# Kernel optimization log

Measured on AMD Instinct MI355X. Metric: run time of the kernel, lower is better.

The kernel has to match this reference:

```python
import jax, jax.numpy as jnp
import numpy as np

B, D0, D1, D2 = 512, 4096, 4096, 4096
W_SCALE = 0.01  # small init so sigmoids stay in a useful range


def setup_inputs() -> dict:
    key = jax.random.key(0)
    k0, k1, k2, k3, k4 = jax.random.split(key, 5)
    return {
        "data": jax.random.uniform(k0, (B, D0), dtype=jnp.float32),
        "W1": jax.random.normal(k1, (D0, D1), dtype=jnp.float32) * W_SCALE,
        "W2": jax.random.normal(k2, (D1, D2), dtype=jnp.float32) * W_SCALE,
        "b1": jax.random.normal(k3, (D1,), dtype=jnp.float32),
        "b2": jax.random.normal(k4, (D2,), dtype=jnp.float32),
        "iterations": 10,
    }


def reference(data, W1, W2, b1, b2, iterations):
    """Mean-field conditional sample of a 3-layer DBM (visible clamped to data).

    Faithful to conditional_sample_general_meanfield with mean_cond (sigmoid
    of bias + interaction), sample_state[0]=False, invtemperature=1.0.
    Schedule per iteration: odd layers (j=1) then even layers (j=2).
    """
    beta = jnp.float32(1.0)
    nb = data.shape[0]
    # initial states: layer mean activations broadcast over the batch
    s1 = jnp.broadcast_to(jax.nn.sigmoid(b1), (nb, b1.shape[0]))
    s2 = jnp.broadcast_to(jax.nn.sigmoid(b2), (nb, b2.shape[0]))

    def gibbs_step(carry, _):
        s1, s2 = carry
        # j=1: interaction from below (gradOutput: data @ W1) and above (gradInput: s2 @ W2^T)
        s1 = jax.nn.sigmoid(b1 + beta * (data @ W1 + s2 @ W2.T))
        # j=2: interaction from below (gradOutput: s1 @ W2); j=0 clamped
        s2 = jax.nn.sigmoid(b2 + beta * (s1 @ W2))
        return (s1, s2), None

    (s1, s2), _ = jax.lax.scan(gibbs_step, (s1, s2), None, length=iterations)
    # original returns [state0, state1, state2]; state0 == data (clamped)
    return jnp.stack([s1, s2])  # [2, B, D]
```

## Files before the change

### kernel.cpp

```cpp
#include <hip/hip_runtime.h>


typedef __bf16 bf16_t;
typedef __attribute__((ext_vector_type(8))) __bf16 bf16x8;
typedef __attribute__((ext_vector_type(4))) float f32x4;
typedef __attribute__((ext_vector_type(2))) _Float16 half2v;

typedef const __attribute__((address_space(1))) void* gptr_t;
typedef __attribute__((address_space(3))) void* lptr_t;

constexpr int M = 512, N = 4096, K = 4096;
constexpr int BM = 128, BN = 128, BK = 32, SUB = 2;
constexpr int SPLIT = 4;
constexpr int PHASES = K / (SPLIT * BK * SUB);
constexpr int NTILES = (M / BM) * (N / BN);
constexpr int TILE_H2 = BM * BN / 2;


__global__ __launch_bounds__(256) void prep_w(const float* __restrict__ in,
                                              bf16_t* __restrict__ outT,
                                              bf16_t* __restrict__ outC) {
  __shared__ float tile[32][65];
  const int tid = threadIdx.x;
  const int x0 = blockIdx.x * 32;
  const int y0 = blockIdx.y * 64;
  const int tx = tid & 31, ty = tid >> 5;
#pragma unroll
  for (int i = 0; i < 8; ++i)
    tile[tx][ty + 8 * i] = in[(size_t)(y0 + ty + 8 * i) * 4096 + x0 + tx];
  __syncthreads();
  {
    const int rr = tid >> 3, seg = tid & 7;
    bf16x8 v;
#pragma unroll
    for (int j = 0; j < 8; ++j) v[j] = (bf16_t)tile[rr][seg * 8 + j];
    *(bf16x8*)(outT + (size_t)(x0 + rr) * 4096 + y0 + seg * 8) = v;
  }
  if (outC) {
    const int yy = tid >> 2, seg = tid & 3;
    bf16x8 v;
#pragma unroll
    for (int j = 0; j < 8; ++j) v[j] = (bf16_t)tile[seg * 8 + j][yy];
    *(bf16x8*)(outC + (size_t)(y0 + yy) * 4096 + x0 + seg * 8) = v;
  }
}

__global__ __launch_bounds__(256) void cvt_bf16(const float* __restrict__ in,
                                                bf16_t* __restrict__ out) {
  const size_t i8 = ((size_t)blockIdx.x * 256 + threadIdx.x) * 8;
  float4 a = *(const float4*)(in + i8);
  float4 b = *(const float4*)(in + i8 + 4);
  bf16x8 o;
  o[0] = (bf16_t)a.x; o[1] = (bf16_t)a.y; o[2] = (bf16_t)a.z; o[3] = (bf16_t)a.w;
  o[4] = (bf16_t)b.x; o[5] = (bf16_t)b.y; o[6] = (bf16_t)b.z; o[7] = (bf16_t)b.w;
  *(bf16x8*)(out + i8) = o;
}

__global__ __launch_bounds__(256) void init_s2(const float* __restrict__ b2,
                                               bf16_t* __restrict__ s2, int total) {
  int i = blockIdx.x * 256 + threadIdx.x;
  if (i < total) {
    float x = b2[i & (N - 1)];
    s2[i] = (bf16_t)(1.0f / (1.0f + __expf(-x)));
  }
}

__global__ __launch_bounds__(256, 2) void gemm_bt(
    const bf16_t* __restrict__ A,
    const bf16_t* __restrict__ BT,
    _Float16* __restrict__ slabs) {
  __shared__ __align__(16) bf16_t sA[2 * SUB * BM * BK];
  __shared__ __align__(16) bf16_t sB[2 * SUB * BN * BK];

  const int tid = threadIdx.x;
  const int wid = tid >> 6;
  const int l   = tid & 63;
  const int r   = l & 15;
  const int q   = l >> 4;
  const int wm  = wid & 1;
  const int wn  = wid >> 1;

  const int m0 = blockIdx.y * BM;
  const int n0 = blockIdx.x * BN;
  const int z  = blockIdx.z;
  const int tile = blockIdx.y * gridDim.x + blockIdx.x;

  const bf16_t* Ab = A + (size_t)m0 * K + (size_t)z * (PHASES * SUB * BK);
  const bf16_t* Bb = BT + (size_t)n0 * K + (size_t)z * (PHASES * SUB * BK);

  const int srow = l >> 2;
  const int scol = (l & 3) * 8;

  f32x4 acc[4][4];
  const f32x4 zero = {0.0f, 0.0f, 0.0f, 0.0f};
#pragma unroll
  for (int i = 0; i < 4; ++i)
#pragma unroll
    for (int j = 0; j < 4; ++j) acc[i][j] = zero;

  auto issue = [&](int ph, int pb) {
    const size_t kof = (size_t)ph * (SUB * BK);
#pragma unroll
    for (int s = 0; s < SUB; ++s) {
#pragma unroll
      for (int cc = 0; cc < 2; ++cc) {
        const int c = wid + cc * 4;
        __builtin_amdgcn_global_load_lds(
            (gptr_t)(Ab + (size_t)(c * 16 + srow) * K + kof + s * BK + scol),
            (lptr_t)(sA + (pb * SUB + s) * 4096 + c * 512), 16, 0, 0);
        __builtin_amdgcn_global_load_lds(
            (gptr_t)(Bb + (size_t)(c * 16 + srow) * K + kof + s * BK + scol),
            (lptr_t)(sB + (pb * SUB + s) * 4096 + c * 512), 16, 0, 0);
      }
    }
  };

  issue(0, 0);
  for (int ph = 0; ph < PHASES; ++ph) {
    const int pb = ph & 1;
    __syncthreads();
    if (ph + 1 < PHASES) issue(ph + 1, pb ^ 1);

#pragma unroll
    for (int s = 0; s < SUB; ++s) {
      const bf16_t* pa = sA + (pb * SUB + s) * 4096;
      const bf16_t* pbuf = sB + (pb * SUB + s) * 4096;
      bf16x8 af[4], bfr[4];
#pragma unroll
      for (int mt = 0; mt < 4; ++mt)
        af[mt] = *(const bf16x8*)(pa + (wm * 64 + mt * 16 + r) * BK + q * 8);
#pragma unroll
      for (int nt = 0; nt < 4; ++nt)
        bfr[nt] = *(const bf16x8*)(pbuf + (wn * 64 + nt * 16 + r) * BK + q * 8);
#pragma unroll
      for (int mt = 0; mt < 4; ++mt)
#pragma unroll
        for (int nt = 0; nt < 4; ++nt)
          acc[mt][nt] = __builtin_amdgcn_mfma_f32_16x16x32_bf16(
              af[mt], bfr[nt], acc[mt][nt], 0, 0, 0);
    }
  }

  half2v* P2 = (half2v*)slabs + ((size_t)z * NTILES + tile) * TILE_H2;
#pragma unroll
  for (int mt = 0; mt < 4; ++mt)
#pragma unroll
    for (int nt = 0; nt < 4; ++nt)
#pragma unroll
      for (int i2 = 0; i2 < 2; ++i2) {
        half2v h;
        h[0] = (_Float16)acc[mt][nt][2 * i2];
        h[1] = (_Float16)acc[mt][nt][2 * i2 + 1];
        P2[((((wid * 4 + mt) * 4 + nt) * 2 + i2)) * 64 + l] = h;
      }
}

template <int MODE>
__global__ __launch_bounds__(256) void epi(const _Float16* __restrict__ slabs,
                                           const float* __restrict__ bias,
                                           const bf16_t* __restrict__ C0b,
                                           bf16_t* __restrict__ outb,
                                           float* __restrict__ outf) {
  const int t = blockIdx.x * 256 + threadIdx.x;
  const int tile = t >> 13;
  const int s = t & 8191;
  float v0 = 0.0f, v1 = 0.0f;
#pragma unroll
  for (int z = 0; z < SPLIT; ++z) {
    half2v h = ((const half2v*)slabs)[((size_t)z * NTILES + tile) * TILE_H2 + s];
    v0 += (float)h[0];
    v1 += (float)h[1];
  }
  const int l = s & 63, i2 = (s >> 6) & 1, nt = (s >> 7) & 3, mt = (s >> 9) & 3,
            wid = s >> 11;
  const int q = l >> 4, r = l & 15, wm = wid & 1, wn = wid >> 1;
  const int row = (tile >> 5) * 128 + wm * 64 + mt * 16 + q * 4 + 2 * i2;
  const int col = (tile & 31) * 128 + wn * 64 + nt * 16 + r;
  const size_t i0 = (size_t)row * N + col;
  const size_t i1 = i0 + N;
  if (MODE == 0) {
    outb[i0] = (bf16_t)v0;
    outb[i1] = (bf16_t)v1;
    return;
  }
  const float bv = bias[col];
  v0 += bv; v1 += bv;
  if (MODE == 1) {
    v0 += (float)C0b[i0];
    v1 += (float)C0b[i1];
  }
  const float s0 = 1.0f / (1.0f + __expf(-v0));
  const float s1 = 1.0f / (1.0f + __expf(-v1));
  outb[i0] = (bf16_t)s0;
  outb[i1] = (bf16_t)s1;
  if (outf) {
    outf[i0] = s0;
    outf[i1] = s1;
  }
}


extern "C" void kernel_launch(void* const* d_in, const int* in_sizes, int n_in,
                              void* d_out, int out_size, void* d_ws, size_t ws_size,
                              hipStream_t stream) {
  const float* data = (const float*)d_in[0];
  const float* W1   = (const float*)d_in[1];
  const float* W2   = (const float*)d_in[2];
  const float* b1   = (const float*)d_in[3];
  const float* b2   = (const float*)d_in[4];

  char* p = (char*)d_ws;
  bf16_t* W1T = (bf16_t*)p; p += (size_t)K * N * 2;
  bf16_t* W2b = (bf16_t*)p; p += (size_t)K * N * 2;
  bf16_t* W2T = (bf16_t*)p; p += (size_t)K * N * 2;
  bf16_t* C0b = (bf16_t*)p; p += (size_t)M * N * 2;
  bf16_t* s1b = (bf16_t*)p; p += (size_t)M * N * 2;
  bf16_t* s2b = (bf16_t*)p; p += (size_t)M * N * 2;
  bf16_t* dat = (bf16_t*)p; p += (size_t)M * K * 2;

  _Float16* slabC = (_Float16*)W2T;
  _Float16* slab  = (_Float16*)W1T;

  float* out_s1 = (float*)d_out;
  float* out_s2 = out_s1 + (size_t)M * N;

  cvt_bf16<<<(M * K) / 2048, 256, 0, stream>>>(data, dat);
  prep_w<<<dim3(128, 64), 256, 0, stream>>>(W1, W1T, (bf16_t*)nullptr);

  dim3 gg(N / BN, M / BM, SPLIT);
  const int epiblocks = (M * N / 2) / 256;

  gemm_bt<<<gg, 256, 0, stream>>>(dat, W1T, slabC);
  epi<0><<<epiblocks, 256, 0, stream>>>(slabC, nullptr, nullptr, C0b, nullptr);

  prep_w<<<dim3(128, 64), 256, 0, stream>>>(W2, W2T, W2b);
  init_s2<<<(M * N) / 256, 256, 0, stream>>>(b2, s2b, M * N);

  for (int it = 0; it < 10; ++it) {
    const bool last = (it == 9);
    gemm_bt<<<gg, 256, 0, stream>>>(s2b, W2b, slab);
    epi<1><<<epiblocks, 256, 0, stream>>>(slab, b1, C0b, s1b,
                                          last ? out_s1 : (float*)nullptr);
    gemm_bt<<<gg, 256, 0, stream>>>(s1b, W2T, slab);
    epi<2><<<epiblocks, 256, 0, stream>>>(slab, b2, nullptr, s2b,
                                          last ? out_s2 : (float*)nullptr);
  }
}
```

Before: 914.9 us.

## Double split-K, shrink LDS stage for higher occupancy, swizzle GEMM block order

The GEMM now uses 8-way split-K with a single BK=32 stage per double-buffered phase, in place of two sub-stages. That halves shared memory so launch bounds can ask for 4 blocks per CU. The grid becomes 1D with a remapping that groups blocks sharing A rows and K slices, aiming for better L2 reuse. The weight transpose kernel moves to 64x64 tiles with float4 loads. The cost is that the epilogue must read and sum twice as many fp16 partial slabs, and shorter K loops with more barriers per FLOP.

```diff
diff --git a/kernel.cpp b/kernel.cpp
--- a/kernel.cpp
+++ b/kernel.cpp
@@ -10,9 +10,9 @@
 typedef __attribute__((address_space(3))) void* lptr_t;
 
 constexpr int M = 512, N = 4096, K = 4096;
-constexpr int BM = 128, BN = 128, BK = 32, SUB = 2;
-constexpr int SPLIT = 4;
-constexpr int PHASES = K / (SPLIT * BK * SUB);
+constexpr int BM = 128, BN = 128, BK = 32;
+constexpr int SPLIT = 8;
+constexpr int PHASES = K / (SPLIT * BK);
 constexpr int NTILES = (M / BM) * (N / BN);
 constexpr int TILE_H2 = BM * BN / 2;
 
@@ -20,28 +20,40 @@
 __global__ __launch_bounds__(256) void prep_w(const float* __restrict__ in,
                                               bf16_t* __restrict__ outT,
                                               bf16_t* __restrict__ outC) {
-  __shared__ float tile[32][65];
+  __shared__ float t[64][65];
   const int tid = threadIdx.x;
-  const int x0 = blockIdx.x * 32;
-  const int y0 = blockIdx.y * 64;
-  const int tx = tid & 31, ty = tid >> 5;
-#pragma unroll
-  for (int i = 0; i < 8; ++i)
-    tile[tx][ty + 8 * i] = in[(size_t)(y0 + ty + 8 * i) * 4096 + x0 + tx];
+  const int x0 = blockIdx.x * 64, y0 = blockIdx.y * 64;
+  const int row = tid >> 4;
+  const int xs  = tid & 15;
+#pragma unroll
+  for (int i = 0; i < 4; ++i) {
+    const int r = row + 16 * i;
+    float4 v = *(const float4*)(in + (size_t)(y0 + r) * 4096 + x0 + xs * 4);
+    t[xs * 4 + 0][r] = v.x;
+    t[xs * 4 + 1][r] = v.y;
+    t[xs * 4 + 2][r] = v.z;
+    t[xs * 4 + 3][r] = v.w;
+  }
   __syncthreads();
-  {
-    const int rr = tid >> 3, seg = tid & 7;
+#pragma unroll
+  for (int j = 0; j < 2; ++j) {
+    const int idx = tid + 256 * j;
+    const int xr = idx >> 3, sg = idx & 7;
     bf16x8 v;
 #pragma unroll
-    for (int j = 0; j < 8; ++j) v[j] = (bf16_t)tile[rr][seg * 8 + j];
-    *(bf16x8*)(outT + (size_t)(x0 + rr) * 4096 + y0 + seg * 8) = v;
+    for (int e = 0; e < 8; ++e) v[e] = (bf16_t)t[xr][sg * 8 + e];
+    *(bf16x8*)(outT + (size_t)(x0 + xr) * 4096 + y0 + sg * 8) = v;
   }
   if (outC) {
-    const int yy = tid >> 2, seg = tid & 3;
-    bf16x8 v;
-#pragma unroll
-    for (int j = 0; j < 8; ++j) v[j] = (bf16_t)tile[seg * 8 + j][yy];
-    *(bf16x8*)(outC + (size_t)(y0 + yy) * 4096 + x0 + seg * 8) = v;
+#pragma unroll
+    for (int j = 0; j < 2; ++j) {
+      const int idx = tid + 256 * j;
+      const int yr = idx >> 3, sg = idx & 7;
+      bf16x8 v;
+#pragma unroll
+      for (int e = 0; e < 8; ++e) v[e] = (bf16_t)t[sg * 8 + e][yr];
+      *(bf16x8*)(outC + (size_t)(y0 + yr) * 4096 + x0 + sg * 8) = v;
+    }
   }
 }
 
@@ -65,12 +77,19 @@
   }
 }
 
-__global__ __launch_bounds__(256, 2) void gemm_bt(
+__global__ __launch_bounds__(256, 4) void gemm_bt(
     const bf16_t* __restrict__ A,
     const bf16_t* __restrict__ BT,
     _Float16* __restrict__ slabs) {
-  __shared__ __align__(16) bf16_t sA[2 * SUB * BM * BK];
-  __shared__ __align__(16) bf16_t sB[2 * SUB * BN * BK];
+  __shared__ __align__(16) bf16_t sA[2 * BM * BK];
+  __shared__ __align__(16) bf16_t sB[2 * BN * BK];
+
+  const int gid = blockIdx.x;
+  const int g = gid >> 5, rr5 = gid & 31;
+  const int y = rr5 >> 3, c = rr5 & 7;
+  const int txz = g * 8 + c;
+  const int x = txz & 31, z = txz >> 5;
+  const int tile = y * 32 + x;
 
   const int tid = threadIdx.x;
   const int wid = tid >> 6;
@@ -80,13 +99,11 @@
   const int wm  = wid & 1;
   const int wn  = wid >> 1;
 
-  const int m0 = blockIdx.y * BM;
-  const int n0 = blockIdx.x * BN;
-  const int z  = blockIdx.z;
-  const int tile = blockIdx.y * gridDim.x + blockIdx.x;
-
-  const bf16_t* Ab = A + (size_t)m0 * K + (size_t)z * (PHASES * SUB * BK);
-  const bf16_t* Bb = BT + (size_t)n0 * K + (size_t)z * (PHASES * SUB * BK);
+  const int m0 = y * BM;
+  const int n0 = x * BN;
+
+  const bf16_t* Ab = A + (size_t)m0 * K + (size_t)z * (PHASES * BK);
+  const bf16_t* Bb = BT + (size_t)n0 * K + (size_t)z * (PHASES * BK);
 
   const int srow = l >> 2;
   const int scol = (l & 3) * 8;
@@ -99,19 +116,16 @@
     for (int j = 0; j < 4; ++j) acc[i][j] = zero;
 
   auto issue = [&](int ph, int pb) {
-    const size_t kof = (size_t)ph * (SUB * BK);
-#pragma unroll
-    for (int s = 0; s < SUB; ++s) {
-#pragma unroll
-      for (int cc = 0; cc < 2; ++cc) {
-        const int c = wid + cc * 4;
-        __builtin_amdgcn_global_load_lds(
-            (gptr_t)(Ab + (size_t)(c * 16 + srow) * K + kof + s * BK + scol),
-            (lptr_t)(sA + (pb * SUB + s) * 4096 + c * 512), 16, 0, 0);
-        __builtin_amdgcn_global_load_lds(
-            (gptr_t)(Bb + (size_t)(c * 16 + srow) * K + kof + s * BK + scol),
-            (lptr_t)(sB + (pb * SUB + s) * 4096 + c * 512), 16, 0, 0);
-      }
+    const size_t kof = (size_t)ph * BK;
+#pragma unroll
+    for (int cc = 0; cc < 2; ++cc) {
+      const int ch = wid + cc * 4;
+      __builtin_amdgcn_global_load_lds(
+          (gptr_t)(Ab + (size_t)(ch * 16 + srow) * K + kof + scol),
+          (lptr_t)(sA + pb * 4096 + ch * 512), 16, 0, 0);
+      __builtin_amdgcn_global_load_lds(
+          (gptr_t)(Bb + (size_t)(ch * 16 + srow) * K + kof + scol),
+          (lptr_t)(sB + pb * 4096 + ch * 512), 16, 0, 0);
     }
   };
 
@@ -121,24 +135,20 @@
     __syncthreads();
     if (ph + 1 < PHASES) issue(ph + 1, pb ^ 1);
 
-#pragma unroll
-    for (int s = 0; s < SUB; ++s) {
-      const bf16_t* pa = sA + (pb * SUB + s) * 4096;
-      const bf16_t* pbuf = sB + (pb * SUB + s) * 4096;
-      bf16x8 af[4], bfr[4];
-#pragma unroll
-      for (int mt = 0; mt < 4; ++mt)
-        af[mt] = *(const bf16x8*)(pa + (wm * 64 + mt * 16 + r) * BK + q * 8);
+    bf16x8 af[4], bfr[4];
+#pragma unroll
+    for (int mt = 0; mt < 4; ++mt)
+      af[mt] = *(const bf16x8*)(sA + pb * 4096 + (wm * 64 + mt * 16 + r) * BK + q * 8);
+#pragma unroll
+    for (int nt = 0; nt < 4; ++nt)
+      bfr[nt] = *(const bf16x8*)(sB + pb * 4096 + (wn * 64 + nt * 16 + r) * BK + q * 8);
+
+#pragma unroll
+    for (int mt = 0; mt < 4; ++mt)
 #pragma unroll
       for (int nt = 0; nt < 4; ++nt)
-        bfr[nt] = *(const bf16x8*)(pbuf + (wn * 64 + nt * 16 + r) * BK + q * 8);
-#pragma unroll
-      for (int mt = 0; mt < 4; ++mt)
-#pragma unroll
-        for (int nt = 0; nt < 4; ++nt)
-          acc[mt][nt] = __builtin_amdgcn_mfma_f32_16x16x32_bf16(
-              af[mt], bfr[nt], acc[mt][nt], 0, 0, 0);
-    }
+        acc[mt][nt] = __builtin_amdgcn_mfma_f32_16x16x32_bf16(
+            af[mt], bfr[nt], acc[mt][nt], 0, 0, 0);
   }
 
   half2v* P2 = (half2v*)slabs + ((size_t)z * NTILES + tile) * TILE_H2;
@@ -151,7 +161,7 @@
         half2v h;
         h[0] = (_Float16)acc[mt][nt][2 * i2];
         h[1] = (_Float16)acc[mt][nt][2 * i2 + 1];
-        P2[((((wid * 4 + mt) * 4 + nt) * 2 + i2)) * 64 + l] = h;
+        P2[(((wid * 4 + mt) * 4 + nt) * 2 + i2) * 64 + l] = h;
       }
 }
 
@@ -225,23 +235,23 @@
   float* out_s2 = out_s1 + (size_t)M * N;
 
   cvt_bf16<<<(M * K) / 2048, 256, 0, stream>>>(data, dat);
-  prep_w<<<dim3(128, 64), 256, 0, stream>>>(W1, W1T, (bf16_t*)nullptr);
-
-  dim3 gg(N / BN, M / BM, SPLIT);
+  prep_w<<<dim3(64, 64), 256, 0, stream>>>(W1, W1T, (bf16_t*)nullptr);
+
+  const int gblocks = 32 * 4 * SPLIT;
   const int epiblocks = (M * N / 2) / 256;
 
-  gemm_bt<<<gg, 256, 0, stream>>>(dat, W1T, slabC);
+  gemm_bt<<<gblocks, 256, 0, stream>>>(dat, W1T, slabC);
   epi<0><<<epiblocks, 256, 0, stream>>>(slabC, nullptr, nullptr, C0b, nullptr);
 
-  prep_w<<<dim3(128, 64), 256, 0, stream>>>(W2, W2T, W2b);
+  prep_w<<<dim3(64, 64), 256, 0, stream>>>(W2, W2T, W2b);
   init_s2<<<(M * N) / 256, 256, 0, stream>>>(b2, s2b, M * N);
 
   for (int it = 0; it < 10; ++it) {
     const bool last = (it == 9);
-    gemm_bt<<<gg, 256, 0, stream>>>(s2b, W2b, slab);
+    gemm_bt<<<gblocks, 256, 0, stream>>>(s2b, W2b, slab);
     epi<1><<<epiblocks, 256, 0, stream>>>(slab, b1, C0b, s1b,
                                           last ? out_s1 : (float*)nullptr);
-    gemm_bt<<<gg, 256, 0, stream>>>(s1b, W2T, slab);
+    gemm_bt<<<gblocks, 256, 0, stream>>>(s1b, W2T, slab);
     epi<2><<<epiblocks, 256, 0, stream>>>(slab, b2, nullptr, s2b,
                                           last ? out_s2 : (float*)nullptr);
   }
```

After: 906.4 us. Within noise of the previous version (-0.9%).
